# Kernel tuning notes

Hardware: AMD Instinct MI355X
Metric: run time of the kernel (lower is better)

The kernel has to match this reference:

```python
import jax, jax.numpy as jnp
import numpy as np

B, T, C, HS = 8, 2048, 1024, 64


def setup_inputs() -> dict:
    key = jax.random.key(0)
    ks = jax.random.split(key, 4)
    x = jax.random.normal(ks[0], (B, T, C), dtype=jnp.float32)
    Wq = jax.random.normal(ks[1], (C, HS), dtype=jnp.float32) * (C ** -0.5)
    Wk = jax.random.normal(ks[2], (C, HS), dtype=jnp.float32) * (C ** -0.5)
    Wv = jax.random.normal(ks[3], (C, HS), dtype=jnp.float32) * (C ** -0.5)
    mask = jnp.tril(jnp.ones((T, T), dtype=jnp.int32))  # causal mask
    return {"x": x, "mask": mask, "Wq": Wq, "Wk": Wk, "Wv": Wv}


def reference(x, mask, Wq, Wk, Wv):
    # x: [B,T,C]; bias-free projections to head_size
    q = jnp.einsum("btc,ch->bth", x, Wq)
    k = jnp.einsum("btc,ch->bth", x, Wk)
    v = jnp.einsum("btc,ch->bth", x, Wv)
    # NOTE: original scales by C**-0.5 (n_embd), not head_size**-0.5
    wei = jnp.einsum("bth,bsh->bts", q, k) * (x.shape[-1] ** -0.5)
    wei = jnp.where(mask[None, :, :] == 0, -jnp.inf, wei)
    wei = jax.nn.softmax(wei, axis=-1)
    # dropout is identity in eval / p=0
    out = jnp.einsum("bts,bsh->bth", wei, v)
    return out
```

## Files before the change

### kernel.cpp

```cpp
#include <hip/hip_runtime.h>
#include <hip/hip_bf16.h>


#define B_  8
#define T_  2048
#define C_  1024
#define HS_ 64
#define MROWS (B_ * T_)

typedef __attribute__((ext_vector_type(8))) short bf16x8;
typedef __attribute__((ext_vector_type(4))) float f32x4;
typedef __attribute__((ext_vector_type(4))) float float4v;

#define SCALE_LOG2 0.04508422037445829f

__device__ __forceinline__ short f2bs(float f) {
    __hip_bfloat16 h = __float2bfloat16(f);
    short s;
    __builtin_memcpy(&s, &h, 2);
    return s;
}

__global__ __launch_bounds__(256) void wt_kernel(
    const float* __restrict__ Wq,
    const float* __restrict__ Wk,
    const float* __restrict__ Wv,
    __hip_bfloat16* __restrict__ Wt) {
    __shared__ float tile[64][65];
    const int m  = blockIdx.x >> 4;
    const int r0 = (blockIdx.x & 15) * 64;
    const float* W = (m == 0) ? Wq : (m == 1) ? Wk : Wv;
    const int i = threadIdx.x >> 6;
    const int j = threadIdx.x & 63;
#pragma unroll
    for (int p = 0; p < 16; ++p) {
        int r = p * 4 + i;
        tile[r][j] = W[(size_t)(r0 + r) * HS_ + j];
    }
    __syncthreads();
#pragma unroll
    for (int p = 0; p < 16; ++p) {
        int h = p * 4 + i;
        Wt[(size_t)m * (HS_ * C_) + (size_t)h * C_ + r0 + j] =
            __float2bfloat16(tile[j][h]);
    }
}

__global__ __launch_bounds__(256, 2) void proj_kernel(
    const float* __restrict__ x,
    const __hip_bfloat16* __restrict__ Wt,
    __hip_bfloat16* __restrict__ Q,
    __hip_bfloat16* __restrict__ Kp,
    __hip_bfloat16* __restrict__ Vt)
{
    __shared__ float xt0[32 * 68];
    __shared__ float xt1[32 * 68];

    const int lane = threadIdx.x & 63;
    const int wave = threadIdx.x >> 6;
    const int quad = lane >> 4;
    const int l15  = lane & 15;
    const int row0 = blockIdx.x * 32;

    const float* gsrc[8];
#pragma unroll
    for (int rr = 0; rr < 8; ++rr)
        gsrc[rr] = x + (size_t)(row0 + wave * 8 + rr) * C_ + lane;

    const __hip_bfloat16* wbase[3];
#pragma unroll
    for (int j = 0; j < 3; ++j) {
        int nt = wave * 3 + j;
        int h  = ((nt & 3) * 16) + l15;
        wbase[j] = Wt + (size_t)(nt >> 2) * (HS_ * C_) + (size_t)h * C_ + quad * 8;
    }

    f32x4 acc[2][3];
#pragma unroll
    for (int rt = 0; rt < 2; ++rt)
#pragma unroll
        for (int j = 0; j < 3; ++j)
            acc[rt][j] = (f32x4){0.f, 0.f, 0.f, 0.f};

    bf16x8 bfr0[2][3], bfr1[2][3];

#define ISSUE_DMA(XT, kc)                                                    \
    do {                                                                     \
        _Pragma("unroll")                                                    \
        for (int rr = 0; rr < 8; ++rr)                                       \
            __builtin_amdgcn_global_load_lds(                                \
                (const __attribute__((address_space(1))) unsigned*)          \
                    (gsrc[rr] + (kc)),                                       \
                (__attribute__((address_space(3))) unsigned*)                \
                    (&XT[(wave * 8 + rr) * 68]),                             \
                4, 0, 0);                                                    \
    } while (0)

#define LOAD_B(BF, kc)                                                       \
    do {                                                                     \
        _Pragma("unroll")                                                    \
        for (int ks = 0; ks < 2; ++ks)                                       \
            _Pragma("unroll")                                                \
            for (int j = 0; j < 3; ++j)                                      \
                BF[ks][j] = *(const bf16x8*)(wbase[j] + (kc) + ks * 32);     \
    } while (0)

#define COMPUTE(XT, BF)                                                      \
    do {                                                                     \
        _Pragma("unroll")                                                    \
        for (int ks = 0; ks < 2; ++ks) {                                     \
            bf16x8 a[2];                                                     \
            _Pragma("unroll")                                                \
            for (int rt = 0; rt < 2; ++rt) {                                 \
                const float4v* p = (const float4v*)                          \
                    &XT[(rt * 16 + l15) * 68 + ks * 32 + quad * 8];          \
                float4v f0 = p[0], f1 = p[1];                                \
                _Pragma("unroll")                                            \
                for (int e = 0; e < 4; ++e) {                                \
                    a[rt][e]     = f2bs(f0[e]);                              \
                    a[rt][4 + e] = f2bs(f1[e]);                              \
                }                                                            \
            }                                                                \
            _Pragma("unroll")                                                \
            for (int rt = 0; rt < 2; ++rt)                                   \
                _Pragma("unroll")                                            \
                for (int j = 0; j < 3; ++j)                                  \
                    acc[rt][j] = __builtin_amdgcn_mfma_f32_16x16x32_bf16(    \
                        a[rt], BF[ks][j], acc[rt][j], 0, 0, 0);              \
        }                                                                    \
    } while (0)

    ISSUE_DMA(xt0, 0);
    LOAD_B(bfr0, 0);

#pragma unroll 1
    for (int kc = 0; kc < C_; kc += 128) {
        __syncthreads();
        if (kc + 64 < C_) {
            ISSUE_DMA(xt1, kc + 64);
            LOAD_B(bfr1, kc + 64);
        }
        COMPUTE(xt0, bfr0);
        __syncthreads();
        if (kc + 128 < C_) {
            ISSUE_DMA(xt0, kc + 128);
            LOAD_B(bfr0, kc + 128);
        }
        COMPUTE(xt1, bfr1);
    }
#undef ISSUE_DMA
#undef LOAD_B
#undef COMPUTE

#pragma unroll
    for (int rt = 0; rt < 2; ++rt) {
#pragma unroll
        for (int j = 0; j < 3; ++j) {
            int nt  = wave * 3 + j;
            int mtx = nt >> 2;
            int col = (nt & 3) * 16 + l15;
#pragma unroll
            for (int r = 0; r < 4; ++r) {
                int row = row0 + rt * 16 + quad * 4 + r;
                __hip_bfloat16 v = __float2bfloat16(acc[rt][j][r]);
                if (mtx == 0) {
                    Q[(size_t)row * HS_ + col] = v;
                } else if (mtx == 1) {
                    Kp[(size_t)row * HS_ + col] = v;
                } else {
                    int bidx = row >> 11;
                    int t    = row & 2047;
                    Vt[((size_t)bidx * HS_ + col) * T_ + t] = v;
                }
            }
        }
    }
}

__global__ __launch_bounds__(256, 2) void attn_kernel(
    const __hip_bfloat16* __restrict__ Q,
    const __hip_bfloat16* __restrict__ Kp,
    const __hip_bfloat16* __restrict__ Vt,
    float* __restrict__ out)
{
    __shared__ __align__(16) __hip_bfloat16 plds[4][32 * 64];
    __shared__ float o_lds[4][32][64];
    __shared__ float l_lds[4][32][16];

    const int tid  = threadIdx.x;
    const int wv   = tid >> 6;
    const int lane = tid & 63;
    const int quad = lane >> 4;
    const int l15  = lane & 15;
    const int b    = blockIdx.x & 7;
    const int lt   = 63 - (blockIdx.x >> 3);
    const int qb   = lt * 32;
    const int rowg = b * T_ + qb;

    bf16x8 qf[2][2];
#pragma unroll
    for (int rt = 0; rt < 2; ++rt)
#pragma unroll
        for (int h = 0; h < 2; ++h)
            qf[rt][h] = *(const bf16x8*)
                (Q + (size_t)(rowg + rt * 16 + l15) * HS_ + h * 32 + quad * 8);

    f32x4 o[2][4];
#pragma unroll
    for (int rt = 0; rt < 2; ++rt)
#pragma unroll
        for (int j = 0; j < 4; ++j) o[rt][j] = (f32x4){0.f, 0.f, 0.f, 0.f};
    float lp[2][4] = {{0.f,0.f,0.f,0.f},{0.f,0.f,0.f,0.f}};

    __hip_bfloat16* pb = plds[wv];
    const int nt = (qb + 31) / 64 + 1;

#define LOADK(KF, kb_)                                                       \
    do {                                                                     \
        const __hip_bfloat16* Kb_ = Kp + (size_t)(b * T_ + (kb_)) * HS_;     \
        _Pragma("unroll")                                                    \
        for (int c = 0; c < 4; ++c)                                          \
            _Pragma("unroll")                                                \
            for (int h = 0; h < 2; ++h)                                      \
                KF[c][h] = *(const bf16x8*)                                  \
                    (Kb_ + (size_t)(c * 16 + l15) * HS_ + h * 32 + quad * 8);\
    } while (0)

#define PROC(KF, kb_)                                                        \
    do {                                                                     \
        bf16x8 vf[2][4];                                                     \
        _Pragma("unroll")                                                    \
        for (int h = 0; h < 2; ++h)                                          \
            _Pragma("unroll")                                                \
            for (int j = 0; j < 4; ++j)                                      \
                vf[h][j] = *(const bf16x8*)                                  \
                    (Vt + ((size_t)b * HS_ + j * 16 + l15) * T_ +            \
                     (kb_) + h * 32 + quad * 8);                             \
        f32x4 s[2][4];                                                       \
        _Pragma("unroll")                                                    \
        for (int rt = 0; rt < 2; ++rt)                                       \
            _Pragma("unroll")                                                \
            for (int c = 0; c < 4; ++c) {                                    \
                s[rt][c] = (f32x4){0.f, 0.f, 0.f, 0.f};                      \
                s[rt][c] = __builtin_amdgcn_mfma_f32_16x16x32_bf16(          \
                    qf[rt][0], KF[c][0], s[rt][c], 0, 0, 0);                 \
                s[rt][c] = __builtin_amdgcn_mfma_f32_16x16x32_bf16(          \
                    qf[rt][1], KF[c][1], s[rt][c], 0, 0, 0);                 \
            }                                                                \
        const bool msk = ((kb_) + 63 > qb);                                  \
        _Pragma("unroll")                                                    \
        for (int rt = 0; rt < 2; ++rt)                                       \
            _Pragma("unroll")                                                \
            for (int c = 0; c < 4; ++c)                                      \
                _Pragma("unroll")                                            \
                for (int r = 0; r < 4; ++r) {                                \
                    float pv = exp2f(s[rt][c][r] * SCALE_LOG2);              \
                    if (msk) {                                               \
                        int row = qb + rt * 16 + quad * 4 + r;               \
                        if ((kb_) + c * 16 + l15 > row) pv = 0.f;            \
                    }                                                        \
                    lp[rt][r] += pv;                                         \
                    pb[(rt * 16 + quad * 4 + r) * 64 + c * 16 + l15] =       \
                        __float2bfloat16(pv);                                \
                }                                                            \
        asm volatile("s_waitcnt lgkmcnt(0)" ::: "memory");                   \
        _Pragma("unroll")                                                    \
        for (int rt = 0; rt < 2; ++rt) {                                     \
            bf16x8 pf0 = *(const bf16x8*)                                    \
                (pb + (rt * 16 + l15) * 64 + quad * 8);                      \
            bf16x8 pf1 = *(const bf16x8*)                                    \
                (pb + (rt * 16 + l15) * 64 + 32 + quad * 8);                 \
            _Pragma("unroll")                                                \
            for (int j = 0; j < 4; ++j) {                                    \
                o[rt][j] = __builtin_amdgcn_mfma_f32_16x16x32_bf16(          \
                    pf0, vf[0][j], o[rt][j], 0, 0, 0);                       \
                o[rt][j] = __builtin_amdgcn_mfma_f32_16x16x32_bf16(          \
                    pf1, vf[1][j], o[rt][j], 0, 0, 0);                       \
            }                                                                \
        }                                                                    \
    } while (0)

    bf16x8 kA[4][2], kB[4][2];
    if (wv < nt) LOADK(kA, wv * 64);
    int i = 0;
#pragma unroll 1
    for (; wv + 4 * (i + 1) < nt; i += 2) {
        LOADK(kB, (wv + 4 * (i + 1)) * 64);
        PROC(kA, (wv + 4 * i) * 64);
        if (wv + 4 * (i + 2) < nt) LOADK(kA, (wv + 4 * (i + 2)) * 64);
        PROC(kB, (wv + 4 * (i + 1)) * 64);
    }
    if (wv + 4 * i < nt) PROC(kA, (wv + 4 * i) * 64);
#undef LOADK
#undef PROC

#pragma unroll
    for (int rt = 0; rt < 2; ++rt) {
#pragma unroll
        for (int j = 0; j < 4; ++j)
#pragma unroll
            for (int r = 0; r < 4; ++r)
                o_lds[wv][rt * 16 + quad * 4 + r][j * 16 + l15] = o[rt][j][r];
#pragma unroll
        for (int r = 0; r < 4; ++r)
            l_lds[wv][rt * 16 + quad * 4 + r][l15] = lp[rt][r];
    }
    __syncthreads();

    if (tid < 32) {
        float s = 0.f;
#pragma unroll
        for (int w = 0; w < 4; ++w)
            for (int c = 0; c < 16; ++c) s += l_lds[w][tid][c];
        l_lds[0][tid][0] = 1.0f / s;
    }
    __syncthreads();

    const int h = tid & 63;
#pragma unroll
    for (int k = 0; k < 8; ++k) {
        int row = (tid >> 6) * 8 + k;
        float s = o_lds[0][row][h] + o_lds[1][row][h] +
                  o_lds[2][row][h] + o_lds[3][row][h];
        out[(size_t)(rowg + row) * HS_ + h] = s * l_lds[0][row][0];
    }
}

extern "C" void kernel_launch(void* const* d_in, const int* in_sizes, int n_in,
                              void* d_out, int out_size, void* d_ws, size_t ws_size,
                              hipStream_t stream) {
    (void)in_sizes; (void)n_in; (void)out_size; (void)ws_size;
    const float* x  = (const float*)d_in[0];
    const float* Wq = (const float*)d_in[2];
    const float* Wk = (const float*)d_in[3];
    const float* Wv = (const float*)d_in[4];

    __hip_bfloat16* ws = (__hip_bfloat16*)d_ws;
    __hip_bfloat16* Wt = ws;
    __hip_bfloat16* Q  = ws + 196608;
    __hip_bfloat16* Kp = ws + 196608 + 1048576;
    __hip_bfloat16* Vt = ws + 196608 + 2 * 1048576;

    wt_kernel<<<48, 256, 0, stream>>>(Wq, Wk, Wv, Wt);
    proj_kernel<<<MROWS / 32, 256, 0, stream>>>(x, Wt, Q, Kp, Vt);
    attn_kernel<<<(T_ / 32) * B_, 256, 0, stream>>>(Q, Kp, Vt, (float*)d_out);
}
```

Before: 152.7 us.

## Swizzle projection LDS tiles, fold softmax scale into Q, pad attention LDS

The projection kernel now loads x tiles with 16-byte global_load_lds transfers into an XOR-swizzled 64-wide LDS layout, replacing 4-byte loads into a padded 68-wide layout. The softmax scale (log2 units) is folded into Q when it is written out, so attention uses a raw hardware exp2. The attention kernel's P, O and L LDS buffers get padded strides to avoid bank conflicts. Query tiles are ordered so that long and short causal blocks interleave for load balance. Pre-scaling Q before bf16 rounding slightly changes numerics, and the extra padding raises LDS use.

```diff
diff --git a/kernel.cpp b/kernel.cpp
--- a/kernel.cpp
+++ b/kernel.cpp
@@ -53,8 +53,8 @@
     __hip_bfloat16* __restrict__ Kp,
     __hip_bfloat16* __restrict__ Vt)
 {
-    __shared__ float xt0[32 * 68];
-    __shared__ float xt1[32 * 68];
+    __shared__ float xt0[32 * 64];
+    __shared__ float xt1[32 * 64];
 
     const int lane = threadIdx.x & 63;
     const int wave = threadIdx.x >> 6;
@@ -62,10 +62,14 @@
     const int l15  = lane & 15;
     const int row0 = blockIdx.x * 32;
 
-    const float* gsrc[8];
-#pragma unroll
-    for (int rr = 0; rr < 8; ++rr)
-        gsrc[rr] = x + (size_t)(row0 + wave * 8 + rr) * C_ + lane;
+    const int u16  = lane & 15;
+    const int rsub = lane >> 4;
+    const float* gsrc[2];
+#pragma unroll
+    for (int h = 0; h < 2; ++h) {
+        int rl = wave * 8 + h * 4 + rsub;
+        gsrc[h] = x + (size_t)(row0 + rl) * C_ + ((u16 ^ (rl & 7)) << 2);
+    }
 
     const __hip_bfloat16* wbase[3];
 #pragma unroll
@@ -87,13 +91,13 @@
 #define ISSUE_DMA(XT, kc)                                                    \
     do {                                                                     \
         _Pragma("unroll")                                                    \
-        for (int rr = 0; rr < 8; ++rr)                                       \
+        for (int hh = 0; hh < 2; ++hh)                                       \
             __builtin_amdgcn_global_load_lds(                                \
                 (const __attribute__((address_space(1))) unsigned*)          \
-                    (gsrc[rr] + (kc)),                                       \
+                    (gsrc[hh] + (kc)),                                       \
                 (__attribute__((address_space(3))) unsigned*)                \
-                    (&XT[(wave * 8 + rr) * 68]),                             \
-                4, 0, 0);                                                    \
+                    (&XT[(wave * 8 + hh * 4) * 64]),                         \
+                16, 0, 0);                                                   \
     } while (0)
 
 #define LOAD_B(BF, kc)                                                       \
@@ -112,9 +116,11 @@
             bf16x8 a[2];                                                     \
             _Pragma("unroll")                                                \
             for (int rt = 0; rt < 2; ++rt) {                                 \
-                const float4v* p = (const float4v*)                          \
-                    &XT[(rt * 16 + l15) * 68 + ks * 32 + quad * 8];          \
-                float4v f0 = p[0], f1 = p[1];                                \
+                const float4v* bp =                                          \
+                    (const float4v*)&XT[(rt * 16 + l15) * 64];               \
+                const int sw_ = l15 & 7;                                     \
+                float4v f0 = bp[(ks * 8 + quad * 2) ^ sw_];                  \
+                float4v f1 = bp[(ks * 8 + quad * 2 + 1) ^ sw_];              \
                 _Pragma("unroll")                                            \
                 for (int e = 0; e < 4; ++e) {                                \
                     a[rt][e]     = f2bs(f0[e]);                              \
@@ -162,15 +168,17 @@
 #pragma unroll
             for (int r = 0; r < 4; ++r) {
                 int row = row0 + rt * 16 + quad * 4 + r;
-                __hip_bfloat16 v = __float2bfloat16(acc[rt][j][r]);
+                float av = acc[rt][j][r];
                 if (mtx == 0) {
-                    Q[(size_t)row * HS_ + col] = v;
+                    Q[(size_t)row * HS_ + col] =
+                        __float2bfloat16(av * SCALE_LOG2);
                 } else if (mtx == 1) {
-                    Kp[(size_t)row * HS_ + col] = v;
+                    Kp[(size_t)row * HS_ + col] = __float2bfloat16(av);
                 } else {
                     int bidx = row >> 11;
                     int t    = row & 2047;
-                    Vt[((size_t)bidx * HS_ + col) * T_ + t] = v;
+                    Vt[((size_t)bidx * HS_ + col) * T_ + t] =
+                        __float2bfloat16(av);
                 }
             }
         }
@@ -183,9 +191,9 @@
     const __hip_bfloat16* __restrict__ Vt,
     float* __restrict__ out)
 {
-    __shared__ __align__(16) __hip_bfloat16 plds[4][32 * 64];
-    __shared__ float o_lds[4][32][64];
-    __shared__ float l_lds[4][32][16];
+    __shared__ __align__(16) __hip_bfloat16 plds[4][32 * 72];
+    __shared__ float o_lds[4][32][65];
+    __shared__ float l_lds[4][32][17];
 
     const int tid  = threadIdx.x;
     const int wv   = tid >> 6;
@@ -193,7 +201,8 @@
     const int quad = lane >> 4;
     const int l15  = lane & 15;
     const int b    = blockIdx.x & 7;
-    const int lt   = 63 - (blockIdx.x >> 3);
+    const int idx  = blockIdx.x >> 3;
+    const int lt   = (idx < 32) ? (63 - idx) : (idx - 32);
     const int qb   = lt * 32;
     const int rowg = b * T_ + qb;
 
@@ -254,22 +263,22 @@
             for (int c = 0; c < 4; ++c)                                      \
                 _Pragma("unroll")                                            \
                 for (int r = 0; r < 4; ++r) {                                \
-                    float pv = exp2f(s[rt][c][r] * SCALE_LOG2);              \
+                    float pv = __builtin_amdgcn_exp2f(s[rt][c][r]);          \
                     if (msk) {                                               \
                         int row = qb + rt * 16 + quad * 4 + r;               \
                         if ((kb_) + c * 16 + l15 > row) pv = 0.f;            \
                     }                                                        \
                     lp[rt][r] += pv;                                         \
-                    pb[(rt * 16 + quad * 4 + r) * 64 + c * 16 + l15] =       \
+                    pb[(rt * 16 + quad * 4 + r) * 72 + c * 16 + l15] =       \
                         __float2bfloat16(pv);                                \
                 }                                                            \
         asm volatile("s_waitcnt lgkmcnt(0)" ::: "memory");                   \
         _Pragma("unroll")                                                    \
         for (int rt = 0; rt < 2; ++rt) {                                     \
             bf16x8 pf0 = *(const bf16x8*)                                    \
-                (pb + (rt * 16 + l15) * 64 + quad * 8);                      \
+                (pb + (rt * 16 + l15) * 72 + quad * 8);                      \
             bf16x8 pf1 = *(const bf16x8*)                                    \
-                (pb + (rt * 16 + l15) * 64 + 32 + quad * 8);                 \
+                (pb + (rt * 16 + l15) * 72 + 32 + quad * 8);                 \
             _Pragma("unroll")                                                \
             for (int j = 0; j < 4; ++j) {                                    \
                 o[rt][j] = __builtin_amdgcn_mfma_f32_16x16x32_bf16(          \
```

Result: faster. 145.6 us (-4.7%).
